# Performance work log

Hardware: AMD Instinct MI355X
Metric: run time of the kernel (lower is better)

The kernel has to match this reference:

```python
import jax, jax.numpy as jnp
import numpy as np

H, D = 16, 64  # num_heads, head_dim (d_model = 1024)


def setup_inputs() -> dict:
    key = jax.random.key(0)
    ks = jax.random.split(key, 5)
    B, S, E = 2, 2048, H * D
    scale = 0.02  # keep logits in a sane range
    return {
        "x": jax.random.normal(ks[0], (B, S, E), jnp.float32),
        "Wq": jax.random.normal(ks[1], (E, E), jnp.float32) * scale,
        "bq": jnp.zeros((E,), jnp.float32),
        "Wk": jax.random.normal(ks[2], (E, E), jnp.float32) * scale,
        "bk": jnp.zeros((E,), jnp.float32),
        "Wv": jax.random.normal(ks[3], (E, E), jnp.float32) * scale,
        "bv": jnp.zeros((E,), jnp.float32),
        "Wo": jax.random.normal(ks[4], (E, E), jnp.float32) * scale,
        "bo": jnp.zeros((E,), jnp.float32),
    }


def reference(x, Wq, bq, Wk, bk, Wv, bv, Wo, bo):
    B, S, E = x.shape

    def proj(W, b):
        # torch nn.Linear: x @ W.T + b; then split heads -> [B, H, S, D]
        return (x @ W.T + b).reshape(B, S, H, D).transpose(0, 2, 1, 3)

    q = proj(Wq, bq)
    k = proj(Wk, bk)
    v = proj(Wv, bv)

    # scores [B, H, S, S]; original masks with -inf BEFORE scaling (-inf/scale == -inf)
    att = jnp.einsum("bhqd,bhkd->bhqk", q, k)
    causal = jnp.triu(jnp.ones((S, S), bool), k=1)  # True above diagonal
    att = jnp.where(causal, -jnp.inf, att) * jnp.float32(1.0 / np.sqrt(D))
    att = jax.nn.softmax(att, axis=-1)

    ctx = jnp.einsum("bhqk,bhkd->bhqd", att, v)  # [B, H, S, D]
    ctx = ctx.transpose(0, 2, 1, 3).reshape(B, S, H * D)  # merge heads
    return ctx @ Wo.T + bo
```

## Files before the change

kernel.cpp:

```cpp
#include <hip/hip_runtime.h>
#include <hip/hip_bf16.h>

#define S_LEN 2048
#define NH    16
#define HD    64
#define EMB   1024
#define BATCH 2
#define M_TOT 4096

typedef __attribute__((ext_vector_type(8)))  __bf16   bf16x8;
typedef __attribute__((ext_vector_type(4)))  __bf16   bf16x4;
typedef __attribute__((ext_vector_type(4)))  float    f32x4;
typedef __attribute__((ext_vector_type(16))) float    f32x16;
typedef __attribute__((ext_vector_type(4)))  unsigned u32x4;

static __device__ __forceinline__ unsigned pk2(float a, float b) {
    unsigned short ua = __builtin_bit_cast(unsigned short, (__bf16)a);
    unsigned short ub = __builtin_bit_cast(unsigned short, (__bf16)b);
    return (unsigned)ua | ((unsigned)ub << 16);
}

__global__ __launch_bounds__(256) void cast_all(const float* __restrict__ x,
        const float* __restrict__ wq, const float* __restrict__ wk,
        const float* __restrict__ wv, const float* __restrict__ wo,
        __bf16* __restrict__ xb, __bf16* __restrict__ wqb,
        __bf16* __restrict__ wkb, __bf16* __restrict__ wvb,
        __bf16* __restrict__ wob) {
    int i = blockIdx.x * 256 + threadIdx.x;
    const float* src; __bf16* dst; int j;
    if (i < (1 << 20)) { src = x; dst = xb; j = i; }
    else {
        int t = i - (1 << 20);
        int r = t >> 18;
        j = t & ((1 << 18) - 1);
        src = (r == 0) ? wq : (r == 1) ? wk : (r == 2) ? wv : wo;
        dst = (r == 0) ? wqb : (r == 1) ? wkb : (r == 2) ? wvb : wob;
    }
    f32x4 v = ((const f32x4*)src)[j];
    bf16x4 o;
    o[0] = (__bf16)v[0]; o[1] = (__bf16)v[1];
    o[2] = (__bf16)v[2]; o[3] = (__bf16)v[3];
    ((bf16x4*)dst)[j] = o;
}

__global__ __launch_bounds__(256) void gemm_qkv(const __bf16* __restrict__ A,
        const __bf16* __restrict__ Wq, const __bf16* __restrict__ Wk,
        const __bf16* __restrict__ Wv,
        const float* __restrict__ bq, const float* __restrict__ bk,
        const float* __restrict__ bv,
        __bf16* __restrict__ Qo, __bf16* __restrict__ Ko, __bf16* __restrict__ Vo) {
    __shared__ __bf16 As[128][64];
    __shared__ __bf16 Bs[128][64];

    const int z = blockIdx.z;
    const __bf16* Bw   = (z == 0) ? Wq : (z == 1) ? Wk : Wv;
    const float*  bias = (z == 0) ? bq : (z == 1) ? bk : bv;
    __bf16*       outp = (z == 0) ? Qo : (z == 1) ? Ko : Vo;

    const int tid  = threadIdx.x;
    const int wid  = tid >> 6;
    const int lane = tid & 63;
    const int lrow = lane & 15;
    const int lhi  = lane >> 4;
    const int m0 = blockIdx.y * 128;
    const int n0 = blockIdx.x * 128;
    const int wr = wid >> 1, wc = wid & 1;

    const int lr8 = lane >> 3;
    const int lc8 = (lane & 7) * 8;

    f32x4 acc[4][4];
#pragma unroll
    for (int i = 0; i < 4; ++i)
#pragma unroll
        for (int j = 0; j < 4; ++j)
            acc[i][j] = (f32x4){0.f, 0.f, 0.f, 0.f};

    for (int k0 = 0; k0 < EMB; k0 += 64) {
#pragma unroll
        for (int t = 0; t < 4; ++t) {
            const int row = wid * 32 + t * 8;
            __builtin_amdgcn_global_load_lds(
                (const __attribute__((address_space(1))) void*)&A[(size_t)(m0 + row + lr8) * EMB + k0 + lc8],
                (__attribute__((address_space(3))) void*)&As[row][0], 16, 0, 0);
            __builtin_amdgcn_global_load_lds(
                (const __attribute__((address_space(1))) void*)&Bw[(size_t)(n0 + row + lr8) * EMB + k0 + lc8],
                (__attribute__((address_space(3))) void*)&Bs[row][0], 16, 0, 0);
        }
        __syncthreads();
#pragma unroll
        for (int kk = 0; kk < 2; ++kk) {
            bf16x8 af[4], bfr[4];
#pragma unroll
            for (int i = 0; i < 4; ++i)
                af[i] = *(const bf16x8*)&As[wr * 64 + i * 16 + lrow][kk * 32 + lhi * 8];
#pragma unroll
            for (int j = 0; j < 4; ++j)
                bfr[j] = *(const bf16x8*)&Bs[wc * 64 + j * 16 + lrow][kk * 32 + lhi * 8];
#pragma unroll
            for (int i = 0; i < 4; ++i)
#pragma unroll
                for (int j = 0; j < 4; ++j)
                    acc[i][j] = __builtin_amdgcn_mfma_f32_16x16x32_bf16(af[i], bfr[j], acc[i][j], 0, 0, 0);
        }
        __syncthreads();
    }

#pragma unroll
    for (int i = 0; i < 4; ++i) {
#pragma unroll
        for (int j = 0; j < 4; ++j) {
#pragma unroll
            for (int jj = 0; jj < 4; ++jj) {
                int row = m0 + wr * 64 + i * 16 + lhi * 4 + jj;
                int col = n0 + wc * 64 + j * 16 + lrow;
                float v = acc[i][j][jj] + bias[col];
                int b = row >> 11, s = row & (S_LEN - 1);
                int h = col >> 6,  d = col & (HD - 1);
                size_t idx = (z == 2)
                    ? ((size_t)(b * NH + h) * HD + d) * S_LEN + s
                    : ((size_t)(b * NH + h) * S_LEN + s) * HD + d;
                outp[idx] = (__bf16)v;
            }
        }
    }
}

__global__ __launch_bounds__(256) void gemm_out(const __bf16* __restrict__ A,
        const __bf16* __restrict__ Bw, const float* __restrict__ bias,
        float* __restrict__ outp) {
    __shared__ __bf16 As[128][64];
    __shared__ __bf16 Bs[128][64];

    const int tid  = threadIdx.x;
    const int wid  = tid >> 6;
    const int lane = tid & 63;
    const int lrow = lane & 15;
    const int lhi  = lane >> 4;
    const int m0 = blockIdx.y * 128;
    const int n0 = blockIdx.x * 128;
    const int wr = wid >> 1, wc = wid & 1;
    const int lr8 = lane >> 3;
    const int lc8 = (lane & 7) * 8;

    f32x4 acc[4][4];
#pragma unroll
    for (int i = 0; i < 4; ++i)
#pragma unroll
        for (int j = 0; j < 4; ++j)
            acc[i][j] = (f32x4){0.f, 0.f, 0.f, 0.f};

    for (int k0 = 0; k0 < EMB; k0 += 64) {
#pragma unroll
        for (int t = 0; t < 4; ++t) {
            const int row = wid * 32 + t * 8;
            __builtin_amdgcn_global_load_lds(
                (const __attribute__((address_space(1))) void*)&A[(size_t)(m0 + row + lr8) * EMB + k0 + lc8],
                (__attribute__((address_space(3))) void*)&As[row][0], 16, 0, 0);
            __builtin_amdgcn_global_load_lds(
                (const __attribute__((address_space(1))) void*)&Bw[(size_t)(n0 + row + lr8) * EMB + k0 + lc8],
                (__attribute__((address_space(3))) void*)&Bs[row][0], 16, 0, 0);
        }
        __syncthreads();
#pragma unroll
        for (int kk = 0; kk < 2; ++kk) {
            bf16x8 af[4], bfr[4];
#pragma unroll
            for (int i = 0; i < 4; ++i)
                af[i] = *(const bf16x8*)&As[wr * 64 + i * 16 + lrow][kk * 32 + lhi * 8];
#pragma unroll
            for (int j = 0; j < 4; ++j)
                bfr[j] = *(const bf16x8*)&Bs[wc * 64 + j * 16 + lrow][kk * 32 + lhi * 8];
#pragma unroll
            for (int i = 0; i < 4; ++i)
#pragma unroll
                for (int j = 0; j < 4; ++j)
                    acc[i][j] = __builtin_amdgcn_mfma_f32_16x16x32_bf16(af[i], bfr[j], acc[i][j], 0, 0, 0);
        }
        __syncthreads();
    }

#pragma unroll
    for (int i = 0; i < 4; ++i)
#pragma unroll
        for (int j = 0; j < 4; ++j)
#pragma unroll
            for (int jj = 0; jj < 4; ++jj) {
                int row = m0 + wr * 64 + i * 16 + lhi * 4 + jj;
                int col = n0 + wc * 64 + j * 16 + lrow;
                outp[(size_t)row * EMB + col] = acc[i][j][jj] + bias[col];
            }
}

__global__ __launch_bounds__(256) void attn_kernel(const __bf16* __restrict__ Q,
        const __bf16* __restrict__ K, const __bf16* __restrict__ Vt,
        __bf16* __restrict__ ctx) {
    __shared__ __bf16 Ol[4][32][72];

    const int wid  = threadIdx.x >> 6;
    const int lane = threadIdx.x & 63;
    const int lq   = lane & 31;
    const int hi   = lane >> 5;
    const int bid  = blockIdx.x;
    const int xcd  = bid & 7;
    const int rem  = bid >> 3;
    const int xq   = rem & 15;
    const int bh   = xcd + 8 * (rem >> 4);
    const int qt   = xq + 16 * wid;
    const int q0w  = qt * 32;

    const __bf16* Qh = Q  + (size_t)bh * S_LEN * HD;
    const __bf16* Kh = K  + (size_t)bh * S_LEN * HD;
    const __bf16* Vh = Vt + (size_t)bh * HD * S_LEN;

    bf16x8 qf[4];
#pragma unroll
    for (int ds = 0; ds < 4; ++ds) {
        bf16x8 t = *(const bf16x8*)&Qh[(size_t)(q0w + lq) * HD + ds * 16 + hi * 8];
#pragma unroll
        for (int j = 0; j < 8; ++j) qf[ds][j] = (__bf16)((float)t[j] * 0.125f);
    }

    f32x16 o0, o1;
#pragma unroll
    for (int r = 0; r < 16; ++r) { o0[r] = 0.f; o1[r] = 0.f; }
    float m = -1e30f, l = 0.f;

    const int nkt = qt + 1;

    bf16x8 kf0, kf1, kf2, kf3;
    {
        const __bf16* kp = &Kh[(size_t)lq * HD + hi * 8];
        kf0 = *(const bf16x8*)(kp);      kf1 = *(const bf16x8*)(kp + 16);
        kf2 = *(const bf16x8*)(kp + 32); kf3 = *(const bf16x8*)(kp + 48);
    }

    for (int kt = 0; kt < nkt; ++kt) {
        const int kk0 = kt * 32;

        bf16x8 va0 = *(const bf16x8*)&Vh[(size_t)lq * S_LEN + kk0 + hi * 8];
        bf16x8 vb0 = *(const bf16x8*)&Vh[(size_t)lq * S_LEN + kk0 + 16 + hi * 8];
        bf16x8 va1 = *(const bf16x8*)&Vh[(size_t)(32 + lq) * S_LEN + kk0 + hi * 8];
        bf16x8 vb1 = *(const bf16x8*)&Vh[(size_t)(32 + lq) * S_LEN + kk0 + 16 + hi * 8];

        const int nk0 = (kt + 1 < nkt ? kt + 1 : kt) * 32;
        bf16x8 nkf0, nkf1, nkf2, nkf3;
        {
            const __bf16* kp = &Kh[(size_t)(nk0 + lq) * HD + hi * 8];
            nkf0 = *(const bf16x8*)(kp);      nkf1 = *(const bf16x8*)(kp + 16);
            nkf2 = *(const bf16x8*)(kp + 32); nkf3 = *(const bf16x8*)(kp + 48);
        }

        f32x16 s;
#pragma unroll
        for (int r = 0; r < 16; ++r) s[r] = 0.f;
        s = __builtin_amdgcn_mfma_f32_32x32x16_bf16(kf0, qf[0], s, 0, 0, 0);
        s = __builtin_amdgcn_mfma_f32_32x32x16_bf16(kf1, qf[1], s, 0, 0, 0);
        s = __builtin_amdgcn_mfma_f32_32x32x16_bf16(kf2, qf[2], s, 0, 0, 0);
        s = __builtin_amdgcn_mfma_f32_32x32x16_bf16(kf3, qf[3], s, 0, 0, 0);

        if (kk0 == q0w) {
#pragma unroll
            for (int r = 0; r < 16; ++r) {
                int keyl = (r & 3) + 8 * (r >> 2) + 4 * hi;
                s[r] = (keyl <= lq) ? s[r] : -1e30f;
            }
        }

        float pm = s[0];
#pragma unroll
        for (int r = 1; r < 16; ++r) pm = fmaxf(pm, s[r]);
        pm = fmaxf(pm, __shfl_xor(pm, 32));

        float mn = fmaxf(m, pm);
        float f  = __expf(m - mn);
        m = mn;

        float ps = 0.f;
#pragma unroll
        for (int r = 0; r < 16; ++r) { s[r] = __expf(s[r] - mn); ps += s[r]; }
        ps += __shfl_xor(ps, 32);
        l = l * f + ps;

#pragma unroll
        for (int r = 0; r < 16; ++r) { o0[r] *= f; o1[r] *= f; }

        unsigned w0 = pk2(s[0],  s[1]),  w1 = pk2(s[2],  s[3]);
        unsigned w2 = pk2(s[4],  s[5]),  w3 = pk2(s[6],  s[7]);
        unsigned w4 = pk2(s[8],  s[9]),  w5 = pk2(s[10], s[11]);
        unsigned w6 = pk2(s[12], s[13]), w7 = pk2(s[14], s[15]);

        unsigned e0 = (unsigned)__shfl_xor((int)(hi ? w0 : w2), 32);
        unsigned e1 = (unsigned)__shfl_xor((int)(hi ? w1 : w3), 32);
        unsigned e2 = (unsigned)__shfl_xor((int)(hi ? w4 : w6), 32);
        unsigned e3 = (unsigned)__shfl_xor((int)(hi ? w5 : w7), 32);
        u32x4 pb0, pb1;
        if (hi) { pb0 = (u32x4){e0, e1, w2, w3}; pb1 = (u32x4){e2, e3, w6, w7}; }
        else    { pb0 = (u32x4){w0, w1, e0, e1}; pb1 = (u32x4){w4, w5, e2, e3}; }
        bf16x8 pb0b = __builtin_bit_cast(bf16x8, pb0);
        bf16x8 pb1b = __builtin_bit_cast(bf16x8, pb1);

        o0 = __builtin_amdgcn_mfma_f32_32x32x16_bf16(va0, pb0b, o0, 0, 0, 0);
        o0 = __builtin_amdgcn_mfma_f32_32x32x16_bf16(vb0, pb1b, o0, 0, 0, 0);
        o1 = __builtin_amdgcn_mfma_f32_32x32x16_bf16(va1, pb0b, o1, 0, 0, 0);
        o1 = __builtin_amdgcn_mfma_f32_32x32x16_bf16(vb1, pb1b, o1, 0, 0, 0);

        kf0 = nkf0; kf1 = nkf1; kf2 = nkf2; kf3 = nkf3;
    }

    float inv = 1.f / l;
#pragma unroll
    for (int r = 0; r < 16; ++r) {
        int d0 = (r & 3) + 8 * (r >> 2) + 4 * hi;
        Ol[wid][lq][d0]      = (__bf16)(o0[r] * inv);
        Ol[wid][lq][32 + d0] = (__bf16)(o1[r] * inv);
    }
    asm volatile("s_waitcnt lgkmcnt(0)" ::: "memory");
    __builtin_amdgcn_sched_barrier(0);

    const int b = bh >> 4, h = bh & 15;
#pragma unroll
    for (int p = 0; p < 4; ++p) {
        int q  = (lane >> 3) + p * 8;
        int d8 = (lane & 7) * 8;
        bf16x8 v = *(const bf16x8*)&Ol[wid][q][d8];
        *(bf16x8*)&ctx[((size_t)b * S_LEN + q0w + q) * EMB + h * HD + d8] = v;
    }
}

extern "C" void kernel_launch(void* const* d_in, const int* in_sizes, int n_in,
                              void* d_out, int out_size, void* d_ws, size_t ws_size,
                              hipStream_t stream) {
    const float* x  = (const float*)d_in[0];
    const float* Wq = (const float*)d_in[1];
    const float* bq = (const float*)d_in[2];
    const float* Wk = (const float*)d_in[3];
    const float* bk = (const float*)d_in[4];
    const float* Wv = (const float*)d_in[5];
    const float* bv = (const float*)d_in[6];
    const float* Wo = (const float*)d_in[7];
    const float* bo = (const float*)d_in[8];

    char* ws = (char*)d_ws;
    __bf16* xb  = (__bf16*)(ws);
    __bf16* Wqb = (__bf16*)(ws + ( 8ull << 20));
    __bf16* Wkb = (__bf16*)(ws + (10ull << 20));
    __bf16* Wvb = (__bf16*)(ws + (12ull << 20));
    __bf16* Wob = (__bf16*)(ws + (14ull << 20));
    __bf16* Qb  = (__bf16*)(ws + (16ull << 20));
    __bf16* Kb  = (__bf16*)(ws + (24ull << 20));
    __bf16* Vtb = (__bf16*)(ws + (32ull << 20));
    __bf16* Cb  = (__bf16*)(ws + (40ull << 20));

    cast_all<<<8192, 256, 0, stream>>>(x, Wq, Wk, Wv, Wo, xb, Wqb, Wkb, Wvb, Wob);

    gemm_qkv<<<dim3(EMB / 128, M_TOT / 128, 3), 256, 0, stream>>>(
        xb, Wqb, Wkb, Wvb, bq, bk, bv, Qb, Kb, Vtb);

    attn_kernel<<<dim3(512), 256, 0, stream>>>(Qb, Kb, Vtb, Cb);

    gemm_out<<<dim3(EMB / 128, M_TOT / 128), 256, 0, stream>>>(Cb, Wob, bo, (float*)d_out);
}
```

Measured before the change: 256.0 us.

## Split each query tile's key range across four waves and merge softmax partials

Each block now handles a single 32-row query tile, and its four waves stride over the key tiles. Each wave keeps its own running max, sum and output accumulator. The partials are combined through shared memory with a log-sum-exp rescale before the bf16 context is written. The grid grows from 512 to 2048 blocks and is ordered so the longest causal tiles launch first. This targets load imbalance and low occupancy when one wave walks a whole causal row alone, at the cost of a block-level sync, an fp32 shared-memory merge and waves that sit idle on short tiles.

```diff
diff --git a/kernel.cpp b/kernel.cpp
--- a/kernel.cpp
+++ b/kernel.cpp
@@ -195,7 +195,8 @@
 __global__ __launch_bounds__(256) void attn_kernel(const __bf16* __restrict__ Q,
         const __bf16* __restrict__ K, const __bf16* __restrict__ Vt,
         __bf16* __restrict__ ctx) {
-    __shared__ __bf16 Ol[4][32][72];
+    __shared__ float Of[4][32][65];
+    __shared__ float MLs[4][2][32];
 
     const int wid  = threadIdx.x >> 6;
     const int lane = threadIdx.x & 63;
@@ -203,11 +204,10 @@
     const int hi   = lane >> 5;
     const int bid  = blockIdx.x;
     const int xcd  = bid & 7;
-    const int rem  = bid >> 3;
-    const int xq   = rem & 15;
-    const int bh   = xcd + 8 * (rem >> 4);
-    const int qt   = xq + 16 * wid;
-    const int q0w  = qt * 32;
+    const int idx  = bid >> 3;
+    const int qt   = 63 - (idx & 63);
+    const int bh   = xcd + 8 * (idx >> 6);
+    const int q0   = qt * 32;
 
     const __bf16* Qh = Q  + (size_t)bh * S_LEN * HD;
     const __bf16* Kh = K  + (size_t)bh * S_LEN * HD;
@@ -216,7 +216,7 @@
     bf16x8 qf[4];
 #pragma unroll
     for (int ds = 0; ds < 4; ++ds) {
-        bf16x8 t = *(const bf16x8*)&Qh[(size_t)(q0w + lq) * HD + ds * 16 + hi * 8];
+        bf16x8 t = *(const bf16x8*)&Qh[(size_t)(q0 + lq) * HD + ds * 16 + hi * 8];
 #pragma unroll
         for (int j = 0; j < 8; ++j) qf[ds][j] = (__bf16)((float)t[j] * 0.125f);
     }
@@ -229,13 +229,13 @@
     const int nkt = qt + 1;
 
     bf16x8 kf0, kf1, kf2, kf3;
-    {
-        const __bf16* kp = &Kh[(size_t)lq * HD + hi * 8];
+    if (wid < nkt) {
+        const __bf16* kp = &Kh[(size_t)(wid * 32 + lq) * HD + hi * 8];
         kf0 = *(const bf16x8*)(kp);      kf1 = *(const bf16x8*)(kp + 16);
         kf2 = *(const bf16x8*)(kp + 32); kf3 = *(const bf16x8*)(kp + 48);
     }
 
-    for (int kt = 0; kt < nkt; ++kt) {
+    for (int kt = wid; kt < nkt; kt += 4) {
         const int kk0 = kt * 32;
 
         bf16x8 va0 = *(const bf16x8*)&Vh[(size_t)lq * S_LEN + kk0 + hi * 8];
@@ -243,7 +243,7 @@
         bf16x8 va1 = *(const bf16x8*)&Vh[(size_t)(32 + lq) * S_LEN + kk0 + hi * 8];
         bf16x8 vb1 = *(const bf16x8*)&Vh[(size_t)(32 + lq) * S_LEN + kk0 + 16 + hi * 8];
 
-        const int nk0 = (kt + 1 < nkt ? kt + 1 : kt) * 32;
+        const int nk0 = (kt + 4 < nkt ? kt + 4 : kt) * 32;
         bf16x8 nkf0, nkf1, nkf2, nkf3;
         {
             const __bf16* kp = &Kh[(size_t)(nk0 + lq) * HD + hi * 8];
@@ -259,7 +259,7 @@
         s = __builtin_amdgcn_mfma_f32_32x32x16_bf16(kf2, qf[2], s, 0, 0, 0);
         s = __builtin_amdgcn_mfma_f32_32x32x16_bf16(kf3, qf[3], s, 0, 0, 0);
 
-        if (kk0 == q0w) {
+        if (kk0 == q0) {
 #pragma unroll
             for (int r = 0; r < 16; ++r) {
                 int keyl = (r & 3) + 8 * (r >> 2) + 4 * hi;
@@ -308,23 +308,36 @@
         kf0 = nkf0; kf1 = nkf1; kf2 = nkf2; kf3 = nkf3;
     }
 
-    float inv = 1.f / l;
 #pragma unroll
     for (int r = 0; r < 16; ++r) {
         int d0 = (r & 3) + 8 * (r >> 2) + 4 * hi;
-        Ol[wid][lq][d0]      = (__bf16)(o0[r] * inv);
-        Ol[wid][lq][32 + d0] = (__bf16)(o1[r] * inv);
-    }
-    asm volatile("s_waitcnt lgkmcnt(0)" ::: "memory");
-    __builtin_amdgcn_sched_barrier(0);
-
-    const int b = bh >> 4, h = bh & 15;
-#pragma unroll
-    for (int p = 0; p < 4; ++p) {
-        int q  = (lane >> 3) + p * 8;
-        int d8 = (lane & 7) * 8;
-        bf16x8 v = *(const bf16x8*)&Ol[wid][q][d8];
-        *(bf16x8*)&ctx[((size_t)b * S_LEN + q0w + q) * EMB + h * HD + d8] = v;
+        Of[wid][lq][d0]      = o0[r];
+        Of[wid][lq][32 + d0] = o1[r];
+    }
+    if (lane < 32) { MLs[wid][0][lq] = m; MLs[wid][1][lq] = l; }
+    __syncthreads();
+
+    {
+        const int tq = threadIdx.x >> 3;
+        const int d8 = (threadIdx.x & 7) * 8;
+        float m0_ = MLs[0][0][tq], m1_ = MLs[1][0][tq];
+        float m2_ = MLs[2][0][tq], m3_ = MLs[3][0][tq];
+        float M = fmaxf(fmaxf(m0_, m1_), fmaxf(m2_, m3_));
+        float a0 = __expf(m0_ - M), a1 = __expf(m1_ - M);
+        float a2 = __expf(m2_ - M), a3 = __expf(m3_ - M);
+        float L = MLs[0][1][tq] * a0 + MLs[1][1][tq] * a1
+                + MLs[2][1][tq] * a2 + MLs[3][1][tq] * a3;
+        float invL = 1.f / L;
+        const int b = bh >> 4, h = bh & 15;
+        bf16x8 outv;
+#pragma unroll
+        for (int e = 0; e < 8; ++e) {
+            int d = d8 + e;
+            float v = a0 * Of[0][tq][d] + a1 * Of[1][tq][d]
+                    + a2 * Of[2][tq][d] + a3 * Of[3][tq][d];
+            outv[e] = (__bf16)(v * invL);
+        }
+        *(bf16x8*)&ctx[((size_t)b * S_LEN + q0 + tq) * EMB + h * HD + d8] = outv;
     }
 }
 
@@ -357,7 +370,7 @@
     gemm_qkv<<<dim3(EMB / 128, M_TOT / 128, 3), 256, 0, stream>>>(
         xb, Wqb, Wkb, Wvb, bq, bk, bv, Qb, Kb, Vtb);
 
-    attn_kernel<<<dim3(512), 256, 0, stream>>>(Qb, Kb, Vtb, Cb);
+    attn_kernel<<<dim3(2048), 256, 0, stream>>>(Qb, Kb, Vtb, Cb);
 
     gemm_out<<<dim3(EMB / 128, M_TOT / 128), 256, 0, stream>>>(Cb, Wob, bo, (float*)d_out);
 }
```

Result: no change. 257.4 us (+0.6%).
